# Kernel optimization log

Hardware: AMD Instinct MI355X
Metric: run time of the kernel (lower is better)

## Reference

```python
import jax, jax.numpy as jnp
import numpy as np
import itertools, string

# Weight space: 2-layer MLP params, flattened in dict-key order (W1, W2, b1, b2).
SPECS = [(0, 1), (1, 2), (1,), (2,)]
N = 1024            # size of each permutable dim (perm ids 0,1,2)
C_IN, C_OUT = 16, 16
NUM_TERMS = [9, 10, 7, 6]   # equivariant basis terms per output leaf


def _set_partitions(elems):
    if not elems:
        yield []
        return
    first, rest = elems[0], elems[1:]
    for part in _set_partitions(rest):
        for i in range(len(part)):
            yield part[:i] + [part[i] + [first]] + part[i + 1:]
        yield part + [[first]]


def gen_basis(out_spec, in_spec, out_dims, x):
    """All permutation-equivariant basis maps from x (*in_dims, c) to (*out_dims, c).
    Basis elements <-> set partitions of (in,out) axis positions sharing a perm id:
    in-axes in a block are diagonalized; in-only blocks are summed; mixed blocks copy
    the axis to the matching out position; out-only blocks broadcast."""
    pos = ([('in', a, p) for a, p in enumerate(in_spec)]
           + [('out', a, p) for a, p in enumerate(out_spec)])
    by_pid = {}
    for q in pos:
        by_pid.setdefault(q[2], []).append(q)
    parts = [list(_set_partitions(by_pid[p])) for p in sorted(by_pid)]
    terms = []
    for combo in itertools.product(*parts):
        blocks = [b for part in combo for b in part]
        pos2b = {(q[0], q[1]): bi for bi, b in enumerate(blocks) for q in b}
        L = string.ascii_lowercase
        in_sub = ''.join(L[pos2b[('in', a)]] for a in range(len(in_spec)))
        mixed = [bi for bi, b in enumerate(blocks)
                 if any(q[0] == 'in' for q in b) and any(q[0] == 'out' for q in b)]
        out_sub = ''.join(L[bi] for bi in mixed)
        # diagonal over repeated in-axes, sum over in-only blocks; z = channel axis
        t = jnp.einsum(f'{in_sub}z->{out_sub}z', x)
        targets = [min(q[1] for q in blocks[bi] if q[0] == 'out') for bi in mixed]
        t = jnp.transpose(t, list(np.argsort(targets)) + [len(mixed)])
        st = sorted(targets)
        for ax in range(len(out_dims)):
            if ax not in st:
                t = jnp.expand_dims(t, ax)
        t = jnp.broadcast_to(t, tuple(out_dims) + (x.shape[-1],))
        for b in blocks:  # diagonal-embed blocks with >1 out axis (not hit for MLP specs)
            outs = sorted(q[1] for q in b if q[0] == 'out')
            for a1, a2 in zip(outs, outs[1:]):
                n = out_dims[a1]
                sh = [1] * (len(out_dims) + 1)
                sh[a1] = n; sh[a2] = n
                t = t * jnp.eye(n, dtype=x.dtype).reshape(sh)
        terms.append(t)
    return terms


def _forward(flat, thetas, biases):
    outs = []
    for i in range(len(flat)):
        out_dims = flat[i].shape[:-1]
        acc = jnp.zeros(tuple(out_dims) + (C_OUT,), dtype=flat[i].dtype)
        k = 0
        for j in range(len(flat)):
            for term in gen_basis(SPECS[i], SPECS[j], out_dims, flat[j]):
                acc = acc + jnp.einsum('...i,io->...o', term, thetas[i][k])
                k += 1
        outs.append(acc + biases[i])
    return tuple(outs)


def setup_inputs() -> dict:
    key = jax.random.key(0)
    ks = jax.random.split(key, 12)
    inp = {
        'W1': jax.random.normal(ks[0], (N, N, C_IN), jnp.float32),
        'W2': jax.random.normal(ks[1], (N, N, C_IN), jnp.float32),
        'b1': jax.random.normal(ks[2], (N, C_IN), jnp.float32),
        'b2': jax.random.normal(ks[3], (N, C_IN), jnp.float32),
    }
    for i, k in enumerate(NUM_TERMS):
        scale = (1.0 / (C_IN * k)) ** 0.5
        inp[f'theta_{i}'] = scale * jax.random.normal(ks[4 + i], (k, C_IN, C_OUT), jnp.float32)
        inp[f'bias_{i}'] = jnp.zeros((C_OUT,), jnp.float32)
    return inp


def reference(W1, W2, b1, b2, theta_0, theta_1, theta_2, theta_3,
              bias_0, bias_1, bias_2, bias_3):
    return _forward([W1, W2, b1, b2],
                    [theta_0, theta_1, theta_2, theta_3],
                    [bias_0, bias_1, bias_2, bias_3])
```

## Files before the change

kernel.cpp:

```cpp
#include <hip/hip_runtime.h>

#define NDIM 1024
#define CH 16
#define ROW_F4 4096

typedef float fvec4 __attribute__((ext_vector_type(4)));

__device__ inline float4 f4add(float4 a, float4 b) {
    return make_float4(a.x + b.x, a.y + b.y, a.z + b.z, a.w + b.w);
}
__device__ inline float4 f4zero() { return make_float4(0.f, 0.f, 0.f, 0.f); }

__global__ __launch_bounds__(256) void k_fused(const float* __restrict__ W1,
                                               const float* __restrict__ W2,
                                               float* __restrict__ rowpart,
                                               float* __restrict__ colpart,
                                               float* __restrict__ tiletot) {
    int t  = threadIdx.x;
    int jt = blockIdx.x, it = blockIdx.y, z = blockIdx.z;
    const float4* base = (const float4*)(z ? W2 : W1)
                       + (size_t)it * 8 * ROW_F4 + jt * 256 + t;
    __shared__ float4 tile[8][258];
    __shared__ float4 rtot[32];
    float4 colacc = f4zero();
#pragma unroll
    for (int r = 0; r < 8; ++r) {
        float4 v = base[(size_t)r * ROW_F4];
        colacc = f4add(colacc, v);
        tile[r][t] = v;
    }
    ((float4*)colpart)[(size_t)(z * 128 + it) * 4096 + jt * 256 + t] = colacc;
    __syncthreads();
    if (t < 32) {
        int r = t >> 2, cq = t & 3;
        float4 s = f4zero();
#pragma unroll
        for (int jl = 0; jl < 64; ++jl) s = f4add(s, tile[r][jl * 4 + cq]);
        ((float4*)rowpart)[(size_t)(z * 16 + jt) * 4096 + (it * 8 + r) * 4 + cq] = s;
        rtot[t] = s;
    }
    __syncthreads();
    if (t < 4) {
        float4 s = f4zero();
#pragma unroll
        for (int r = 0; r < 8; ++r) s = f4add(s, rtot[r * 4 + t]);
        ((float4*)tiletot)[(size_t)(z * 2048 + it * 16 + jt) * 4 + t] = s;
    }
}

__global__ __launch_bounds__(256) void k_reduce(const float* __restrict__ rowpart,
                                                const float* __restrict__ colpart,
                                                const float* __restrict__ tiletot,
                                                const float* __restrict__ b1,
                                                const float* __restrict__ b2,
                                                float* __restrict__ rowsumF,
                                                float* __restrict__ colsumF,
                                                float* __restrict__ sums) {
    int t = threadIdx.x;
    int b = blockIdx.x;
    if (b < 128) {
        const float4* cp = (const float4*)colpart;
        int o = b * 64 + (t & 63);
        int p = t >> 6;
        int z = o >> 12, rem = o & 4095;
        float4 s = f4zero();
#pragma unroll 8
        for (int k = 0; k < 32; ++k)
            s = f4add(s, cp[(size_t)(z * 128 + p * 32 + k) * 4096 + rem]);
        __shared__ float4 lds[256];
        lds[t] = s;
        __syncthreads();
        if (t < 64) {
            float4 r = f4add(f4add(lds[t], lds[t + 64]),
                             f4add(lds[t + 128], lds[t + 192]));
            ((float4*)colsumF)[o] = r;
        }
    } else if (b < 160) {
        const float4* rp = (const float4*)rowpart;
        int o = (b - 128) * 256 + t;
        int z = o >> 12, rem = o & 4095;
        float4 s = f4zero();
#pragma unroll
        for (int k = 0; k < 16; ++k)
            s = f4add(s, rp[(size_t)(z * 16 + k) * 4096 + rem]);
        ((float4*)rowsumF)[o] = s;
    } else if (b == 160) {
        int c = t & 15, p = (t >> 4) & 7, z = t >> 7;
        float s = 0.f;
#pragma unroll 8
        for (int m = 0; m < 256; ++m)
            s += tiletot[(size_t)(z * 2048 + p * 256 + m) * 16 + c];
        __shared__ float ldsA[2][8][16];
        ldsA[z][p][c] = s;
        __syncthreads();
        if (t < 32) {
            int zz = t >> 4, cc = t & 15;
            float r = 0.f;
#pragma unroll
            for (int q = 0; q < 8; ++q) r += ldsA[zz][q][cc];
            sums[zz * 16 + cc] = r;
        }
    } else {
        int w = b - 161;
        const float* src = w ? b2 : b1;
        int c = t & 15, p = t >> 4;
        float s = 0.f;
#pragma unroll 8
        for (int m = 0; m < 64; ++m)
            s += src[(size_t)(p * 64 + m) * 16 + c];
        __shared__ float ldsB[16][16];
        ldsB[p][c] = s;
        __syncthreads();
        if (t < 16) {
            float r = 0.f;
#pragma unroll
            for (int q = 0; q < 16; ++q) r += ldsB[q][t];
            sums[32 + w * 16 + t] = r;
        }
    }
}

__global__ __launch_bounds__(256) void k_smalls(const float* __restrict__ rowsum,
                                                const float* __restrict__ colsum,
                                                const float* __restrict__ sums,
                                                const float* __restrict__ b1,
                                                const float* __restrict__ b2,
                                                const float* __restrict__ th0,
                                                const float* __restrict__ th1,
                                                const float* __restrict__ th2,
                                                const float* __restrict__ th3,
                                                const float* __restrict__ bias0,
                                                const float* __restrict__ bias1,
                                                const float* __restrict__ bias2,
                                                const float* __restrict__ bias3,
                                                float* __restrict__ R0, float* __restrict__ C0,
                                                float* __restrict__ R1, float* __restrict__ C1,
                                                float* __restrict__ out2, float* __restrict__ out3) {
    int gt = blockIdx.x * 256 + threadIdx.x;
    int i = gt >> 4, o = gt & 15;
    const float* rs1 = rowsum + i * 16;
    const float* rs2 = rowsum + 16384 + i * 16;
    const float* cs1 = colsum + i * 16;
    const float* cs2 = colsum + 16384 + i * 16;
    const float* b1i = b1 + i * 16;
    const float* b2i = b2 + i * 16;
    float r0 = 0.f, c0a = 0.f, r1 = 0.f, c1a = 0.f, o2 = 0.f, o3 = 0.f;
    float k0 = 0.f, k1 = 0.f, k2 = 0.f, k3 = 0.f;
#pragma unroll
    for (int c = 0; c < 16; ++c) {
        float sW1 = sums[c], sW2 = sums[16 + c], sb1 = sums[32 + c], sb2 = sums[48 + c];
        r0  += rs1[c] * th0[(1 * 16 + c) * 16 + o];
        c0a += cs1[c] * th0[(2 * 16 + c) * 16 + o]
             + rs2[c] * th0[(4 * 16 + c) * 16 + o]
             + b1i[c] * th0[(6 * 16 + c) * 16 + o];
        k0  += sW1 * th0[(3 * 16 + c) * 16 + o] + sW2 * th0[(5 * 16 + c) * 16 + o]
             + sb1 * th0[(7 * 16 + c) * 16 + o] + sb2 * th0[(8 * 16 + c) * 16 + o];
        r1  += cs1[c] * th1[(0 * 16 + c) * 16 + o]
             + rs2[c] * th1[(3 * 16 + c) * 16 + o]
             + b1i[c] * th1[(6 * 16 + c) * 16 + o];
        c1a += cs2[c] * th1[(4 * 16 + c) * 16 + o]
             + b2i[c] * th1[(8 * 16 + c) * 16 + o];
        k1  += sW1 * th1[(1 * 16 + c) * 16 + o] + sW2 * th1[(5 * 16 + c) * 16 + o]
             + sb1 * th1[(7 * 16 + c) * 16 + o] + sb2 * th1[(9 * 16 + c) * 16 + o];
        o2  += cs1[c] * th2[(0 * 16 + c) * 16 + o]
             + rs2[c] * th2[(2 * 16 + c) * 16 + o]
             + b1i[c] * th2[(4 * 16 + c) * 16 + o];
        k2  += sW1 * th2[(1 * 16 + c) * 16 + o] + sW2 * th2[(3 * 16 + c) * 16 + o]
             + sb1 * th2[(5 * 16 + c) * 16 + o] + sb2 * th2[(6 * 16 + c) * 16 + o];
        o3  += cs2[c] * th3[(1 * 16 + c) * 16 + o]
             + b2i[c] * th3[(4 * 16 + c) * 16 + o];
        k3  += sW1 * th3[(0 * 16 + c) * 16 + o] + sW2 * th3[(2 * 16 + c) * 16 + o]
             + sb1 * th3[(3 * 16 + c) * 16 + o] + sb2 * th3[(5 * 16 + c) * 16 + o];
    }
    R0[gt]   = r0;
    C0[gt]   = c0a + k0 + bias0[o];
    R1[gt]   = r1;
    C1[gt]   = c1a + k1 + bias1[o];
    out2[gt] = o2 + k2 + bias2[o];
    out3[gt] = o3 + k3 + bias3[o];
}

__global__ __launch_bounds__(256) void k_main(const float* __restrict__ W1,
                                              const float* __restrict__ W2,
                                              const float* __restrict__ R0,
                                              const float* __restrict__ C0,
                                              const float* __restrict__ R1,
                                              const float* __restrict__ C1,
                                              const float* __restrict__ th0,
                                              const float* __restrict__ th1,
                                              float* __restrict__ out0,
                                              float* __restrict__ out1) {
    int z = blockIdx.z;
    const float* __restrict__ W  = z ? W2 : W1;
    const float* __restrict__ R  = z ? R1 : R0;
    const float* __restrict__ Cc = z ? C1 : C0;
    const float* __restrict__ TH = z ? th1 : th0;
    float* __restrict__ out      = z ? out1 : out0;

    int t   = threadIdx.x;
    int q   = t & 3;
    int jf4 = blockIdx.x * 256 + t;
    int i0  = blockIdx.y * 16;

    float th_reg[4][4][4];
#pragma unroll
    for (int p = 0; p < 4; ++p)
#pragma unroll
        for (int m = 0; m < 4; ++m) {
            float4 v = *(const float4*)(TH + (4 * (q ^ p) + m) * 16 + 4 * q);
            th_reg[p][m][0] = v.x; th_reg[p][m][1] = v.y;
            th_reg[p][m][2] = v.z; th_reg[p][m][3] = v.w;
        }
    float4 cq = ((const float4*)Cc)[jf4];

    const float4* Wf4 = (const float4*)W;
    fvec4*        Onv = (fvec4*)out;

#pragma unroll 2
    for (int ii = 0; ii < 16; ++ii) {
        int i = i0 + ii;
        float4 x  = Wf4[(size_t)i * 4096 + jf4];
        float4 rr = *(const float4*)(R + i * 16 + 4 * q);
        float acc[4] = {cq.x + rr.x, cq.y + rr.y, cq.z + rr.z, cq.w + rr.w};
        float4 xs[4];
        xs[0] = x;
#pragma unroll
        for (int p = 1; p < 4; ++p) {
            xs[p].x = __shfl_xor(x.x, p);
            xs[p].y = __shfl_xor(x.y, p);
            xs[p].z = __shfl_xor(x.z, p);
            xs[p].w = __shfl_xor(x.w, p);
        }
#pragma unroll
        for (int p = 0; p < 4; ++p) {
            float xm0 = xs[p].x, xm1 = xs[p].y, xm2 = xs[p].z, xm3 = xs[p].w;
#pragma unroll
            for (int k = 0; k < 4; ++k)
                acc[k] += xm0 * th_reg[p][0][k] + xm1 * th_reg[p][1][k]
                        + xm2 * th_reg[p][2][k] + xm3 * th_reg[p][3][k];
        }
        fvec4 val = {acc[0], acc[1], acc[2], acc[3]};
        __builtin_nontemporal_store(val, Onv + (size_t)i * 4096 + jf4);
    }
}

extern "C" void kernel_launch(void* const* d_in, const int* in_sizes, int n_in,
                              void* d_out, int out_size, void* d_ws, size_t ws_size,
                              hipStream_t stream) {
    const float* W1    = (const float*)d_in[0];
    const float* W2    = (const float*)d_in[1];
    const float* b1    = (const float*)d_in[2];
    const float* b2    = (const float*)d_in[3];
    const float* th0   = (const float*)d_in[4];
    const float* bias0 = (const float*)d_in[5];
    const float* th1   = (const float*)d_in[6];
    const float* bias1 = (const float*)d_in[7];
    const float* th2   = (const float*)d_in[8];
    const float* bias2 = (const float*)d_in[9];
    const float* th3   = (const float*)d_in[10];
    const float* bias3 = (const float*)d_in[11];

    float* out  = (float*)d_out;
    float* out0 = out;
    float* out1 = out + (size_t)NDIM * NDIM * CH;
    float* out2 = out1 + (size_t)NDIM * NDIM * CH;
    float* out3 = out2 + (size_t)NDIM * CH;

    float* rowpart = out0;
    float* colpart = out0 + 524288;
    float* tiletot = out0 + 4718592;

    float* ws      = (float*)d_ws;
    float* rowsumF = ws;
    float* colsumF = ws + 32768;
    float* sums    = ws + 65536;
    float* R0      = ws + 65600;
    float* C0      = R0 + 16384;
    float* R1      = C0 + 16384;
    float* C1      = R1 + 16384;

    k_fused<<<dim3(16, 128, 2), dim3(256), 0, stream>>>(W1, W2, rowpart, colpart, tiletot);
    k_reduce<<<dim3(163), dim3(256), 0, stream>>>(rowpart, colpart, tiletot, b1, b2,
                                                  rowsumF, colsumF, sums);
    k_smalls<<<dim3(64), dim3(256), 0, stream>>>(rowsumF, colsumF, sums, b1, b2,
                                                 th0, th1, th2, th3,
                                                 bias0, bias1, bias2, bias3,
                                                 R0, C0, R1, C1, out2, out3);
    k_main<<<dim3(16, 64, 2), dim3(256), 0, stream>>>(W1, W2, R0, C0, R1, C1,
                                                      th0, th1 + 2 * 256,
                                                      out0, out1);
}
```

Measured before the change: 89.69 us.

## Merge reduction stages into one persistent launch with atomic-counter dependencies

Folds the tile-partial, reduce and small-output kernels into a single launch. Later blocks spin on global atomic counters until every producer block has signalled completion, which removes two kernel launch boundaries and their drain gaps. A memset is added to reset the counters before the launch. This depends on blocks being dispatched roughly in index order so that no spinning block starves a producer, and the spinning adds its own latency.

```diff
diff --git a/kernel.cpp b/kernel.cpp
--- a/kernel.cpp
+++ b/kernel.cpp
@@ -6,123 +6,34 @@
 
 typedef float fvec4 __attribute__((ext_vector_type(4)));
 
+#define FUSED_NB  4096
+#define REDUCE_NB 163
+#define SMALLS_NB 64
+
 __device__ inline float4 f4add(float4 a, float4 b) {
     return make_float4(a.x + b.x, a.y + b.y, a.z + b.z, a.w + b.w);
 }
 __device__ inline float4 f4zero() { return make_float4(0.f, 0.f, 0.f, 0.f); }
 
-__global__ __launch_bounds__(256) void k_fused(const float* __restrict__ W1,
-                                               const float* __restrict__ W2,
-                                               float* __restrict__ rowpart,
-                                               float* __restrict__ colpart,
-                                               float* __restrict__ tiletot) {
-    int t  = threadIdx.x;
-    int jt = blockIdx.x, it = blockIdx.y, z = blockIdx.z;
-    const float4* base = (const float4*)(z ? W2 : W1)
-                       + (size_t)it * 8 * ROW_F4 + jt * 256 + t;
-    __shared__ float4 tile[8][258];
-    __shared__ float4 rtot[32];
-    float4 colacc = f4zero();
-#pragma unroll
-    for (int r = 0; r < 8; ++r) {
-        float4 v = base[(size_t)r * ROW_F4];
-        colacc = f4add(colacc, v);
-        tile[r][t] = v;
-    }
-    ((float4*)colpart)[(size_t)(z * 128 + it) * 4096 + jt * 256 + t] = colacc;
+__device__ inline void spin_acquire(unsigned* ctr, unsigned target) {
+    if (threadIdx.x == 0) {
+        while (__hip_atomic_load(ctr, __ATOMIC_ACQUIRE, __HIP_MEMORY_SCOPE_AGENT)
+               != target)
+            __builtin_amdgcn_s_sleep(8);
+        __threadfence();
+    }
     __syncthreads();
-    if (t < 32) {
-        int r = t >> 2, cq = t & 3;
-        float4 s = f4zero();
-#pragma unroll
-        for (int jl = 0; jl < 64; ++jl) s = f4add(s, tile[r][jl * 4 + cq]);
-        ((float4*)rowpart)[(size_t)(z * 16 + jt) * 4096 + (it * 8 + r) * 4 + cq] = s;
-        rtot[t] = s;
-    }
+}
+__device__ inline void signal_release(unsigned* ctr) {
     __syncthreads();
-    if (t < 4) {
-        float4 s = f4zero();
-#pragma unroll
-        for (int r = 0; r < 8; ++r) s = f4add(s, rtot[r * 4 + t]);
-        ((float4*)tiletot)[(size_t)(z * 2048 + it * 16 + jt) * 4 + t] = s;
-    }
-}
-
-__global__ __launch_bounds__(256) void k_reduce(const float* __restrict__ rowpart,
-                                                const float* __restrict__ colpart,
-                                                const float* __restrict__ tiletot,
-                                                const float* __restrict__ b1,
-                                                const float* __restrict__ b2,
-                                                float* __restrict__ rowsumF,
-                                                float* __restrict__ colsumF,
-                                                float* __restrict__ sums) {
-    int t = threadIdx.x;
-    int b = blockIdx.x;
-    if (b < 128) {
-        const float4* cp = (const float4*)colpart;
-        int o = b * 64 + (t & 63);
-        int p = t >> 6;
-        int z = o >> 12, rem = o & 4095;
-        float4 s = f4zero();
-#pragma unroll 8
-        for (int k = 0; k < 32; ++k)
-            s = f4add(s, cp[(size_t)(z * 128 + p * 32 + k) * 4096 + rem]);
-        __shared__ float4 lds[256];
-        lds[t] = s;
-        __syncthreads();
-        if (t < 64) {
-            float4 r = f4add(f4add(lds[t], lds[t + 64]),
-                             f4add(lds[t + 128], lds[t + 192]));
-            ((float4*)colsumF)[o] = r;
-        }
-    } else if (b < 160) {
-        const float4* rp = (const float4*)rowpart;
-        int o = (b - 128) * 256 + t;
-        int z = o >> 12, rem = o & 4095;
-        float4 s = f4zero();
-#pragma unroll
-        for (int k = 0; k < 16; ++k)
-            s = f4add(s, rp[(size_t)(z * 16 + k) * 4096 + rem]);
-        ((float4*)rowsumF)[o] = s;
-    } else if (b == 160) {
-        int c = t & 15, p = (t >> 4) & 7, z = t >> 7;
-        float s = 0.f;
-#pragma unroll 8
-        for (int m = 0; m < 256; ++m)
-            s += tiletot[(size_t)(z * 2048 + p * 256 + m) * 16 + c];
-        __shared__ float ldsA[2][8][16];
-        ldsA[z][p][c] = s;
-        __syncthreads();
-        if (t < 32) {
-            int zz = t >> 4, cc = t & 15;
-            float r = 0.f;
-#pragma unroll
-            for (int q = 0; q < 8; ++q) r += ldsA[zz][q][cc];
-            sums[zz * 16 + cc] = r;
-        }
-    } else {
-        int w = b - 161;
-        const float* src = w ? b2 : b1;
-        int c = t & 15, p = t >> 4;
-        float s = 0.f;
-#pragma unroll 8
-        for (int m = 0; m < 64; ++m)
-            s += src[(size_t)(p * 64 + m) * 16 + c];
-        __shared__ float ldsB[16][16];
-        ldsB[p][c] = s;
-        __syncthreads();
-        if (t < 16) {
-            float r = 0.f;
-#pragma unroll
-            for (int q = 0; q < 16; ++q) r += ldsB[q][t];
-            sums[32 + w * 16 + t] = r;
-        }
-    }
-}
-
-__global__ __launch_bounds__(256) void k_smalls(const float* __restrict__ rowsum,
-                                                const float* __restrict__ colsum,
-                                                const float* __restrict__ sums,
+    if (threadIdx.x == 0) {
+        __threadfence();
+        __hip_atomic_fetch_add(ctr, 1u, __ATOMIC_RELEASE, __HIP_MEMORY_SCOPE_AGENT);
+    }
+}
+
+__global__ __launch_bounds__(256) void k_phase1(const float* __restrict__ W1,
+                                                const float* __restrict__ W2,
                                                 const float* __restrict__ b1,
                                                 const float* __restrict__ b2,
                                                 const float* __restrict__ th0,
@@ -133,15 +44,129 @@
                                                 const float* __restrict__ bias1,
                                                 const float* __restrict__ bias2,
                                                 const float* __restrict__ bias3,
+                                                float* __restrict__ rowpart,
+                                                float* __restrict__ colpart,
+                                                float* __restrict__ tiletot,
+                                                float* __restrict__ rowsumF,
+                                                float* __restrict__ colsumF,
+                                                float* __restrict__ sums,
                                                 float* __restrict__ R0, float* __restrict__ C0,
                                                 float* __restrict__ R1, float* __restrict__ C1,
-                                                float* __restrict__ out2, float* __restrict__ out3) {
-    int gt = blockIdx.x * 256 + threadIdx.x;
+                                                float* __restrict__ out2, float* __restrict__ out3,
+                                                unsigned* __restrict__ ctr) {
+    __shared__ float4 smem[8 * 258 + 32];
+    int t   = threadIdx.x;
+    int bid = blockIdx.x;
+
+    if (bid < FUSED_NB) {
+        int jt = bid & 15, it = (bid >> 4) & 127, z = bid >> 11;
+        const float4* base = (const float4*)(z ? W2 : W1)
+                           + (size_t)it * 8 * ROW_F4 + jt * 256 + t;
+        float4 (*tile)[258] = (float4(*)[258])smem;
+        float4* rtot = smem + 8 * 258;
+        float4 colacc = f4zero();
+#pragma unroll
+        for (int r = 0; r < 8; ++r) {
+            float4 v = base[(size_t)r * ROW_F4];
+            colacc = f4add(colacc, v);
+            tile[r][t] = v;
+        }
+        ((float4*)colpart)[(size_t)(z * 128 + it) * 4096 + jt * 256 + t] = colacc;
+        __syncthreads();
+        if (t < 32) {
+            int r = t >> 2, cq = t & 3;
+            float4 s = f4zero();
+#pragma unroll
+            for (int jl = 0; jl < 64; ++jl) s = f4add(s, tile[r][jl * 4 + cq]);
+            ((float4*)rowpart)[(size_t)(z * 16 + jt) * 4096 + (it * 8 + r) * 4 + cq] = s;
+            rtot[t] = s;
+        }
+        __syncthreads();
+        if (t < 4) {
+            float4 s = f4zero();
+#pragma unroll
+            for (int r = 0; r < 8; ++r) s = f4add(s, rtot[r * 4 + t]);
+            ((float4*)tiletot)[(size_t)(z * 2048 + it * 16 + jt) * 4 + t] = s;
+        }
+        signal_release(&ctr[0]);
+        return;
+    }
+
+    if (bid < FUSED_NB + REDUCE_NB) {
+        int b = bid - FUSED_NB;
+        if (b < 161) spin_acquire(&ctr[0], FUSED_NB);
+        if (b < 128) {
+            const float4* cp = (const float4*)colpart;
+            int o = b * 64 + (t & 63);
+            int p = t >> 6;
+            int z = o >> 12, rem = o & 4095;
+            float4 s = f4zero();
+#pragma unroll 8
+            for (int k = 0; k < 32; ++k)
+                s = f4add(s, cp[(size_t)(z * 128 + p * 32 + k) * 4096 + rem]);
+            float4* lds = smem;
+            lds[t] = s;
+            __syncthreads();
+            if (t < 64) {
+                float4 r = f4add(f4add(lds[t], lds[t + 64]),
+                                 f4add(lds[t + 128], lds[t + 192]));
+                ((float4*)colsumF)[o] = r;
+            }
+        } else if (b < 160) {
+            const float4* rp = (const float4*)rowpart;
+            int o = (b - 128) * 256 + t;
+            int z = o >> 12, rem = o & 4095;
+            float4 s = f4zero();
+#pragma unroll
+            for (int k = 0; k < 16; ++k)
+                s = f4add(s, rp[(size_t)(z * 16 + k) * 4096 + rem]);
+            ((float4*)rowsumF)[o] = s;
+        } else if (b == 160) {
+            int c = t & 15, p = (t >> 4) & 7, z = t >> 7;
+            float s = 0.f;
+#pragma unroll 8
+            for (int m = 0; m < 256; ++m)
+                s += tiletot[(size_t)(z * 2048 + p * 256 + m) * 16 + c];
+            float* ldsA = (float*)smem;
+            ldsA[(z * 8 + p) * 16 + c] = s;
+            __syncthreads();
+            if (t < 32) {
+                int zz = t >> 4, cc = t & 15;
+                float r = 0.f;
+#pragma unroll
+                for (int q = 0; q < 8; ++q) r += ldsA[(zz * 8 + q) * 16 + cc];
+                sums[zz * 16 + cc] = r;
+            }
+        } else {
+            int w = b - 161;
+            const float* src = w ? b2 : b1;
+            int c = t & 15, p = t >> 4;
+            float s = 0.f;
+#pragma unroll 8
+            for (int m = 0; m < 64; ++m)
+                s += src[(size_t)(p * 64 + m) * 16 + c];
+            float* ldsB = (float*)smem;
+            ldsB[p * 16 + c] = s;
+            __syncthreads();
+            if (t < 16) {
+                float r = 0.f;
+#pragma unroll
+                for (int q = 0; q < 16; ++q) r += ldsB[q * 16 + t];
+                sums[32 + w * 16 + t] = r;
+            }
+        }
+        signal_release(&ctr[1]);
+        return;
+    }
+
+    spin_acquire(&ctr[1], REDUCE_NB);
+    int sblk = bid - FUSED_NB - REDUCE_NB;
+    int gt = sblk * 256 + t;
     int i = gt >> 4, o = gt & 15;
-    const float* rs1 = rowsum + i * 16;
-    const float* rs2 = rowsum + 16384 + i * 16;
-    const float* cs1 = colsum + i * 16;
-    const float* cs2 = colsum + 16384 + i * 16;
+    const float* rs1 = rowsumF + i * 16;
+    const float* rs2 = rowsumF + 16384 + i * 16;
+    const float* cs1 = colsumF + i * 16;
+    const float* cs2 = colsumF + 16384 + i * 16;
     const float* b1i = b1 + i * 16;
     const float* b2i = b2 + i * 16;
     float r0 = 0.f, c0a = 0.f, r1 = 0.f, c1a = 0.f, o2 = 0.f, o3 = 0.f;
@@ -278,14 +303,14 @@
     float* C0      = R0 + 16384;
     float* R1      = C0 + 16384;
     float* C1      = R1 + 16384;
-
-    k_fused<<<dim3(16, 128, 2), dim3(256), 0, stream>>>(W1, W2, rowpart, colpart, tiletot);
-    k_reduce<<<dim3(163), dim3(256), 0, stream>>>(rowpart, colpart, tiletot, b1, b2,
-                                                  rowsumF, colsumF, sums);
-    k_smalls<<<dim3(64), dim3(256), 0, stream>>>(rowsumF, colsumF, sums, b1, b2,
-                                                 th0, th1, th2, th3,
-                                                 bias0, bias1, bias2, bias3,
-                                                 R0, C0, R1, C1, out2, out3);
+    unsigned* ctr  = (unsigned*)(ws + 150000);
+
+    hipMemsetAsync(ctr, 0, 2 * sizeof(unsigned), stream);
+
+    k_phase1<<<dim3(FUSED_NB + REDUCE_NB + SMALLS_NB), dim3(256), 0, stream>>>(
+        W1, W2, b1, b2, th0, th1, th2, th3, bias0, bias1, bias2, bias3,
+        rowpart, colpart, tiletot, rowsumF, colsumF, sums,
+        R0, C0, R1, C1, out2, out3, ctr);
     k_main<<<dim3(16, 64, 2), dim3(256), 0, stream>>>(W1, W2, R0, C0, R1, C1,
                                                       th0, th1 + 2 * 256,
                                                       out0, out1);
```

Measured after the change: 295.7 us. 3.3x slower.
